# Kernel optimization log

Hardware: AMD Instinct MI355X
Metric: run time of the kernel (lower is better)

Reference implementation:

```python
import jax, jax.numpy as jnp
import numpy as np

N_NODES = 100000
N_EDGES = 1600000
F_IN = 500
HIDDEN = 64
N_CLASS = 40


def gcn_conv(x, W, b, src, dst, n_nodes):
    """PyG GCNConv: add self-loops, symmetric deg^-1/2 normalization,
    linear transform then scatter-add aggregation at dst."""
    h = x @ W  # [N, out]
    loop = jnp.arange(n_nodes, dtype=src.dtype)
    s = jnp.concatenate([src, loop])  # sources incl. self-loops
    d = jnp.concatenate([dst, loop])
    deg = jax.ops.segment_sum(jnp.ones_like(d, dtype=h.dtype), d, num_segments=n_nodes)
    dinv = jnp.where(deg > 0, jax.lax.rsqrt(deg), 0.0)
    norm = dinv[s] * dinv[d]  # [E+N]
    msg = h[s] * norm[:, None]  # gather + scale, [E+N, out]
    out = jax.ops.segment_sum(msg, d, num_segments=n_nodes)
    return out + b


def setup_inputs() -> dict:
    key = jax.random.key(0)
    k1, k2, k3, k4 = jax.random.split(key, 4)
    x = jax.random.normal(k1, (N_NODES, F_IN), dtype=jnp.float32)
    edge_index = jax.random.randint(k2, (2, N_EDGES), 0, N_NODES, dtype=jnp.int64)
    # Glorot-style init for GCNConv weights
    W1 = jax.random.normal(k3, (F_IN, HIDDEN), dtype=jnp.float32) / np.sqrt(F_IN)
    b1 = jnp.zeros((HIDDEN,), dtype=jnp.float32)
    W2 = jax.random.normal(k4, (HIDDEN, N_CLASS), dtype=jnp.float32) / np.sqrt(HIDDEN)
    b2 = jnp.zeros((N_CLASS,), dtype=jnp.float32)
    return {"x": x, "W1": W1, "b1": b1, "W2": W2, "b2": b2, "edge_index": edge_index}


def reference(x, W1, b1, W2, b2, edge_index):
    src, dst = edge_index[0], edge_index[1]
    n = x.shape[0]
    h = jax.nn.relu(gcn_conv(x, W1, b1, src, dst, n))
    # dropout is identity in eval mode (F.dropout with training=False)
    out = gcn_conv(h, W2, b2, src, dst, n)
    return jax.nn.log_softmax(out, axis=1)
```

## Files before the change

### kernel.cpp

```cpp
#include <hip/hip_runtime.h>
#include <math.h>

#define N_NODES 100000
#define N_EDGES 1600000
#define F_IN    500
#define HIDDEN  64
#define N_CLASS 40
#define KPAD    512

#define NB   2048
#define NPB  49
#define EPB  16384
#define CAP  1536

typedef __attribute__((ext_vector_type(4))) float f32x4;
typedef __attribute__((ext_vector_type(8))) __bf16 bf16x8;

__device__ __forceinline__ unsigned short f2bf(float f) {
    unsigned int u = __float_as_uint(f);
    u = (u + 0x7FFF + ((u >> 16) & 1)) >> 16;
    return (unsigned short)u;
}
__device__ __forceinline__ unsigned int packbf(float a, float b) {
    return (unsigned int)f2bf(a) | ((unsigned int)f2bf(b) << 16);
}
__device__ __forceinline__ float bfu_lo(unsigned int v) {
    return __uint_as_float(v << 16);
}
__device__ __forceinline__ float bfu_hi(unsigned int v) {
    return __uint_as_float(v & 0xFFFF0000u);
}

__global__ void k_prep_w1t(const float* __restrict__ w1, unsigned short* __restrict__ w1t,
                           int* __restrict__ bcnt) {
    int idx = blockIdx.x * blockDim.x + threadIdx.x;
    if (idx < NB) bcnt[idx] = 0;
    if (idx >= HIDDEN * KPAD) return;
    int n = idx >> 9, k = idx & (KPAD - 1);
    float v = (k < F_IN) ? w1[k * HIDDEN + n] : 0.f;
    w1t[idx] = f2bf(v);
}

__launch_bounds__(1024)
__global__ void k_bhist(const int* __restrict__ dst, int* __restrict__ bcnt, int e) {
    __shared__ int h[NB];
    for (int i = threadIdx.x; i < NB; i += 1024) h[i] = 0;
    __syncthreads();
    int base = blockIdx.x * EPB;
#pragma unroll
    for (int j = 0; j < 16; ++j) {
        int i = base + j * 1024 + threadIdx.x;
        if (i < e) atomicAdd(&h[dst[i] / NPB], 1);
    }
    __syncthreads();
    for (int i = threadIdx.x; i < NB; i += 1024)
        if (h[i]) atomicAdd(&bcnt[i], h[i]);
}

__launch_bounds__(1024)
__global__ void k_bscan(const int* __restrict__ bcnt, int* __restrict__ bptr,
                        int* __restrict__ bcur) {
    __shared__ int s[1024];
    int t = threadIdx.x;
    int a = bcnt[2 * t], b = bcnt[2 * t + 1];
    int v = a + b;
    s[t] = v;
    __syncthreads();
    for (int off = 1; off < 1024; off <<= 1) {
        int u = (t >= off) ? s[t - off] : 0;
        __syncthreads();
        s[t] += u;
        __syncthreads();
    }
    int excl = s[t] - v;
    bptr[2 * t] = excl;     bptr[2 * t + 1] = excl + a;
    bcur[2 * t] = excl;     bcur[2 * t + 1] = excl + a;
    if (t == 1023) bptr[NB] = s[1023];
}

__launch_bounds__(1024)
__global__ void k_bfill(const int* __restrict__ src, const int* __restrict__ dst,
                        int* __restrict__ bcur, int2* __restrict__ ebuf, int e) {
    __shared__ int hist[NB];
    __shared__ int base_[NB];
    for (int i = threadIdx.x; i < NB; i += 1024) hist[i] = 0;
    __syncthreads();
    int b0 = blockIdx.x * EPB;
    int s_[16], d_[16];
#pragma unroll
    for (int j = 0; j < 16; ++j) {
        int i = b0 + j * 1024 + threadIdx.x;
        if (i < e) {
            s_[j] = src[i];
            d_[j] = dst[i];
            atomicAdd(&hist[d_[j] / NPB], 1);
        } else d_[j] = -1;
    }
    __syncthreads();
    for (int i = threadIdx.x; i < NB; i += 1024) {
        int hc = hist[i];
        base_[i] = hc ? atomicAdd(&bcur[i], hc) : 0;
        hist[i] = 0;
    }
    __syncthreads();
#pragma unroll
    for (int j = 0; j < 16; ++j) {
        if (d_[j] >= 0) {
            int bu = d_[j] / NPB;
            int r = atomicAdd(&hist[bu], 1);
            ebuf[base_[bu] + r] = make_int2(s_[j], d_[j]);
        }
    }
}

__launch_bounds__(256)
__global__ void k_bucket_csr(const int2* __restrict__ ebuf, const int* __restrict__ bptr,
                             int* __restrict__ rp, int* __restrict__ col,
                             float* __restrict__ dinv, int n) {
    int b  = blockIdx.x;
    int lo = b * NPB;
    if (lo >= n) return;
    int hi  = min(lo + NPB, n);
    int eb0 = bptr[b], ec = bptr[b + 1] - eb0;

    __shared__ int2 pairs[CAP];
    __shared__ int  hist[NPB];
    __shared__ int  excl[NPB + 1];
    for (int j = threadIdx.x; j < NPB; j += 256) hist[j] = 0;
    __syncthreads();
    for (int i = threadIdx.x; i < ec; i += 256) {
        int2 p = ebuf[eb0 + i];
        if (i < CAP) pairs[i] = p;
        atomicAdd(&hist[p.y - lo], 1);
    }
    __syncthreads();
    if (threadIdx.x == 0) {
        int acc = 0;
        for (int j = 0; j < NPB; ++j) { excl[j] = acc; acc += hist[j]; }
        excl[NPB] = acc;
    }
    __syncthreads();
    for (int j = threadIdx.x; j < hi - lo; j += 256) {
        rp[lo + j]   = eb0 + excl[j];
        dinv[lo + j] = rsqrtf((float)(hist[j] + 1));
    }
    if (hi == n && threadIdx.x == 0) rp[n] = eb0 + ec;
    __syncthreads();
    for (int j = threadIdx.x; j < NPB; j += 256) hist[j] = 0;
    __syncthreads();
    for (int i = threadIdx.x; i < ec; i += 256) {
        int2 p  = (i < CAP) ? pairs[i] : ebuf[eb0 + i];
        int  li = p.y - lo;
        int  r  = atomicAdd(&hist[li], 1);
        col[eb0 + excl[li] + r] = p.x;
    }
}

__launch_bounds__(512)
__global__ void k_gemm1(const float* __restrict__ x, const unsigned short* __restrict__ w1t,
                        const float* __restrict__ dinv, unsigned short* __restrict__ hs, int n) {
    constexpr int LDW = 520;
    __shared__ __align__(16) unsigned short w1l[HIDDEN * LDW];

    const int tid  = threadIdx.x;
    const int wave = tid >> 6;
    const int lane = tid & 63;
    const int quad = lane >> 4;
    const int l16  = lane & 15;

    {
        const uint4* g = (const uint4*)w1t;
#pragma unroll
        for (int i = 0; i < 8; ++i) {
            int c   = i * 512 + tid;
            int row = c >> 6, cc = c & 63;
            uint4 v = g[c];
            *(uint4*)&w1l[row * LDW + cc * 8] = v;
        }
    }
    __syncthreads();

    const int rowb = blockIdx.x * 128 + wave * 16;
    const int  row = rowb + l16;
    const bool vr  = row < n;
    const float* p = &x[(size_t)(vr ? row : 0) * F_IN];
    const float4 z4 = make_float4(0.f, 0.f, 0.f, 0.f);

    f32x4 acc[4];
#pragma unroll
    for (int ct = 0; ct < 4; ++ct) acc[ct] = (f32x4)0.f;

    float4 xa[8], xb[8];
    auto XLOAD = [&](int ks) {
        const int c0 = ks * 32 + quad * 8;
        if (ks < 15) {
            xa[ks % 8] = vr ? *(const float4*)&p[c0]     : z4;
            xb[ks % 8] = vr ? *(const float4*)&p[c0 + 4] : z4;
        } else {
            const bool cv0 = (c0 + 4 <= F_IN);
            const bool cv1 = (c0 + 8 <= F_IN);
            xa[ks % 8] = (vr && cv0) ? *(const float4*)&p[c0]     : z4;
            xb[ks % 8] = (vr && cv1) ? *(const float4*)&p[c0 + 4] : z4;
        }
    };
#pragma unroll
    for (int ks = 0; ks < 8; ++ks) XLOAD(ks);

#pragma unroll
    for (int ks = 0; ks < 16; ++ks) {
        bf16x8 bfrag[4];
#pragma unroll
        for (int ct = 0; ct < 4; ++ct)
            bfrag[ct] = *(const bf16x8*)&w1l[(ct * 16 + l16) * LDW + ks * 32 + quad * 8];
        const float4 ca = xa[ks % 8];
        const float4 cb = xb[ks % 8];
        if (ks + 8 < 16) XLOAD(ks + 8);
        union { bf16x8 v; unsigned int u[4]; } af;
        af.u[0] = packbf(ca.x, ca.y); af.u[1] = packbf(ca.z, ca.w);
        af.u[2] = packbf(cb.x, cb.y); af.u[3] = packbf(cb.z, cb.w);
#pragma unroll
        for (int ct = 0; ct < 4; ++ct)
            acc[ct] = __builtin_amdgcn_mfma_f32_16x16x32_bf16(af.v, bfrag[ct], acc[ct], 0, 0, 0);
    }

#pragma unroll
    for (int reg = 0; reg < 4; ++reg) {
        int grow = rowb + quad * 4 + reg;
        if (grow < n) {
            float dv = dinv[grow];
#pragma unroll
            for (int ct = 0; ct < 4; ++ct)
                hs[(size_t)grow * HIDDEN + ct * 16 + l16] = f2bf(dv * acc[ct][reg]);
        }
    }
}

template <int F, bool RELU, bool LSM>
__launch_bounds__(256)
__global__ void k_agg(const uint2* __restrict__ hs2, const int* __restrict__ rp,
                      const int* __restrict__ col, const float* __restrict__ dinv,
                      const float* __restrict__ bias, float* __restrict__ out, int n) {
    constexpr int PW2 = F / 4;
    const int lane = threadIdx.x & 63;
    const int q    = lane >> 4;
    const int p    = lane & 15;
    const bool act = p < PW2;
    int wid = __builtin_amdgcn_readfirstlane((blockIdx.x * blockDim.x + threadIdx.x) >> 6);
    const int nw = (gridDim.x * blockDim.x) >> 6;

    for (; wid < n; wid += nw) {
        const int beg = rp[wid], end = rp[wid + 1];
        float a0 = 0.f, a1 = 0.f, a2 = 0.f, a3 = 0.f;
        int e = beg + q;
        for (; e + 12 < end; e += 16) {
            int c0 = col[e], c1 = col[e + 4], c2 = col[e + 8], c3 = col[e + 12];
            uint2 v0 = act ? hs2[(unsigned)c0 * PW2 + p] : make_uint2(0u, 0u);
            uint2 v1 = act ? hs2[(unsigned)c1 * PW2 + p] : make_uint2(0u, 0u);
            uint2 v2 = act ? hs2[(unsigned)c2 * PW2 + p] : make_uint2(0u, 0u);
            uint2 v3 = act ? hs2[(unsigned)c3 * PW2 + p] : make_uint2(0u, 0u);
            a0 += bfu_lo(v0.x) + bfu_lo(v1.x) + bfu_lo(v2.x) + bfu_lo(v3.x);
            a1 += bfu_hi(v0.x) + bfu_hi(v1.x) + bfu_hi(v2.x) + bfu_hi(v3.x);
            a2 += bfu_lo(v0.y) + bfu_lo(v1.y) + bfu_lo(v2.y) + bfu_lo(v3.y);
            a3 += bfu_hi(v0.y) + bfu_hi(v1.y) + bfu_hi(v2.y) + bfu_hi(v3.y);
        }
        if (e + 4 < end) {
            int c0 = col[e], c1 = col[e + 4];
            uint2 v0 = act ? hs2[(unsigned)c0 * PW2 + p] : make_uint2(0u, 0u);
            uint2 v1 = act ? hs2[(unsigned)c1 * PW2 + p] : make_uint2(0u, 0u);
            a0 += bfu_lo(v0.x) + bfu_lo(v1.x);
            a1 += bfu_hi(v0.x) + bfu_hi(v1.x);
            a2 += bfu_lo(v0.y) + bfu_lo(v1.y);
            a3 += bfu_hi(v0.y) + bfu_hi(v1.y);
            e += 8;
        }
        if (e < end) {
            int c0 = col[e];
            uint2 v0 = act ? hs2[(unsigned)c0 * PW2 + p] : make_uint2(0u, 0u);
            a0 += bfu_lo(v0.x); a1 += bfu_hi(v0.x);
            a2 += bfu_lo(v0.y); a3 += bfu_hi(v0.y);
        }
        a0 += __shfl_xor(a0, 16); a1 += __shfl_xor(a1, 16);
        a2 += __shfl_xor(a2, 16); a3 += __shfl_xor(a3, 16);
        a0 += __shfl_xor(a0, 32); a1 += __shfl_xor(a1, 32);
        a2 += __shfl_xor(a2, 32); a3 += __shfl_xor(a3, 32);

        const float di = dinv[wid];
        uint2 sv  = act ? hs2[(unsigned)wid * PW2 + p] : make_uint2(0u, 0u);
        float4 bv = act ? *(const float4*)&bias[4 * p] : make_float4(0.f, 0.f, 0.f, 0.f);
        float r0 = di * (a0 + bfu_lo(sv.x)) + bv.x;
        float r1 = di * (a1 + bfu_hi(sv.x)) + bv.y;
        float r2 = di * (a2 + bfu_lo(sv.y)) + bv.z;
        float r3 = di * (a3 + bfu_hi(sv.y)) + bv.w;
        if (RELU) {
            r0 = fmaxf(r0, 0.f); r1 = fmaxf(r1, 0.f);
            r2 = fmaxf(r2, 0.f); r3 = fmaxf(r3, 0.f);
        }
        if (LSM) {
            float m = act ? fmaxf(fmaxf(r0, r1), fmaxf(r2, r3)) : -INFINITY;
#pragma unroll
            for (int off = 8; off; off >>= 1) m = fmaxf(m, __shfl_xor(m, off));
            float ex = act ? (__expf(r0 - m) + __expf(r1 - m) + __expf(r2 - m) + __expf(r3 - m))
                           : 0.f;
#pragma unroll
            for (int off = 8; off; off >>= 1) ex += __shfl_xor(ex, off);
            float lse = m + __logf(ex);
            r0 -= lse; r1 -= lse; r2 -= lse; r3 -= lse;
        }
        if (q == 0 && act)
            *(float4*)&out[(size_t)wid * F + 4 * p] = make_float4(r0, r1, r2, r3);
    }
}

__launch_bounds__(256)
__global__ void k_gemm2(const float* __restrict__ a, const float* __restrict__ w,
                        const float* __restrict__ dinv, unsigned short* __restrict__ out, int n) {
    __shared__ float ws[HIDDEN * N_CLASS];
    for (int idx = threadIdx.x; idx < HIDDEN * N_CLASS; idx += 256) ws[idx] = w[idx];
    __syncthreads();
    int idx = blockIdx.x * 256 + threadIdx.x;
    if (idx >= n * N_CLASS) return;
    int i = idx / N_CLASS, j = idx - i * N_CLASS;
    float s = 0.f;
#pragma unroll
    for (int k = 0; k < HIDDEN; k += 4) {
        float4 xv = *(const float4*)&a[(size_t)i * HIDDEN + k];
        s = fmaf(xv.x, ws[k * N_CLASS + j], s);
        s = fmaf(xv.y, ws[(k + 1) * N_CLASS + j], s);
        s = fmaf(xv.z, ws[(k + 2) * N_CLASS + j], s);
        s = fmaf(xv.w, ws[(k + 3) * N_CLASS + j], s);
    }
    out[idx] = f2bf(dinv[i] * s);
}

extern "C" void kernel_launch(void* const* d_in, const int* in_sizes, int n_in,
                              void* d_out, int out_size, void* d_ws, size_t ws_size,
                              hipStream_t stream) {
    const float* x   = (const float*)d_in[0];
    const float* W1  = (const float*)d_in[1];
    const float* b1  = (const float*)d_in[2];
    const float* W2  = (const float*)d_in[3];
    const float* b2  = (const float*)d_in[4];
    const int*   ei  = (const int*)d_in[5];
    const int*   src = ei;
    const int*   dst = ei + N_EDGES;
    float*       out = (float*)d_out;

    char*  ws  = (char*)d_ws;
    size_t off = 0;
    auto alloc = [&](size_t bytes) -> void* {
        void* p = ws + off;
        off += (bytes + 255) & ~(size_t)255;
        return p;
    };
    int*            bcnt = (int*)alloc((size_t)NB * 4);
    int*            bptr = (int*)alloc((size_t)(NB + 1) * 4);
    int*            bcur = (int*)alloc((size_t)NB * 4);
    int*            rp   = (int*)alloc((size_t)(N_NODES + 1) * 4);
    int*            col  = (int*)alloc((size_t)N_EDGES * 4);
    float*          dinv = (float*)alloc((size_t)N_NODES * 4);
    unsigned short* w1t  = (unsigned short*)alloc((size_t)HIDDEN * KPAD * 2);
    unsigned short* h1s  = (unsigned short*)alloc((size_t)N_NODES * HIDDEN * 2);
    float*          h1a  = (float*)alloc((size_t)N_NODES * HIDDEN * 4);
    int2*           ebuf = (int2*)h1a;
    unsigned short* h2s  = h1s;

    const int NBH = (N_EDGES + EPB - 1) / EPB;

    k_prep_w1t<<<(HIDDEN * KPAD + 255) / 256, 256, 0, stream>>>(W1, w1t, bcnt);
    k_bhist<<<NBH, 1024, 0, stream>>>(dst, bcnt, N_EDGES);
    k_bscan<<<1, 1024, 0, stream>>>(bcnt, bptr, bcur);
    k_bfill<<<NBH, 1024, 0, stream>>>(src, dst, bcur, ebuf, N_EDGES);
    k_bucket_csr<<<NB, 256, 0, stream>>>(ebuf, bptr, rp, col, dinv, N_NODES);

    k_gemm1<<<(N_NODES + 127) / 128, 512, 0, stream>>>(x, w1t, dinv, h1s, N_NODES);
    k_agg<HIDDEN, true, false><<<2048, 256, 0, stream>>>(
        (const uint2*)h1s, rp, col, dinv, b1, h1a, N_NODES);

    k_gemm2<<<(N_NODES * N_CLASS + 255) / 256, 256, 0, stream>>>(h1a, W2, dinv, h2s, N_NODES);
    k_agg<N_CLASS, false, true><<<2048, 256, 0, stream>>>(
        (const uint2*)h2s, rp, col, dinv, b2, out, N_NODES);
}
```

Before: 514.2 us.

## Stage x tiles into LDS with direct global-to-LDS loads in triple buffer

```diff
diff --git a/kernel.cpp b/kernel.cpp
--- a/kernel.cpp
+++ b/kernel.cpp
@@ -29,6 +29,11 @@
 }
 __device__ __forceinline__ float bfu_hi(unsigned int v) {
     return __uint_as_float(v & 0xFFFF0000u);
+}
+__device__ __forceinline__ void gload_lds16(const void* g, void* l) {
+    __builtin_amdgcn_global_load_lds(
+        (const __attribute__((address_space(1))) unsigned int*)g,
+        (__attribute__((address_space(3))) unsigned int*)l, 16, 0, 0);
 }
 
 __global__ void k_prep_w1t(const float* __restrict__ w1, unsigned short* __restrict__ w1t,
@@ -161,6 +166,7 @@
                         const float* __restrict__ dinv, unsigned short* __restrict__ hs, int n) {
     constexpr int LDW = 520;
     __shared__ __align__(16) unsigned short w1l[HIDDEN * LDW];
+    __shared__ __align__(16) char xs[3][8][2048];
 
     const int tid  = threadIdx.x;
     const int wave = tid >> 6;
@@ -178,46 +184,78 @@
             *(uint4*)&w1l[row * LDW + cc * 8] = v;
         }
     }
-    __syncthreads();
 
     const int rowb = blockIdx.x * 128 + wave * 16;
-    const int  row = rowb + l16;
-    const bool vr  = row < n;
-    const float* p = &x[(size_t)(vr ? row : 0) * F_IN];
-    const float4 z4 = make_float4(0.f, 0.f, 0.f, 0.f);
+
+    const int rloc = lane >> 3;
+    const int csrc = (lane & 7) ^ rloc;
+    int gr0 = rowb + rloc;      if (gr0 > n - 1) gr0 = n - 1;
+    int gr1 = rowb + 8 + rloc;  if (gr1 > n - 1) gr1 = n - 1;
+    const char* sb0 = (const char*)x + (size_t)gr0 * (F_IN * 4) + csrc * 16;
+    const char* sb1 = (const char*)x + (size_t)gr1 * (F_IN * 4) + csrc * 16;
+
+    auto STAGE = [&](int ks) {
+        char* d = &xs[ks % 3][wave][0];
+        gload_lds16(sb0 + ks * 128, d);
+        gload_lds16(sb1 + ks * 128, d + 1024);
+    };
+
+    STAGE(0); STAGE(1);
+    asm volatile("s_waitcnt vmcnt(0)" ::: "memory");
+    __syncthreads();
 
     f32x4 acc[4];
 #pragma unroll
     for (int ct = 0; ct < 4; ++ct) acc[ct] = (f32x4)0.f;
 
-    float4 xa[8], xb[8];
-    auto XLOAD = [&](int ks) {
-        const int c0 = ks * 32 + quad * 8;
-        if (ks < 15) {
-            xa[ks % 8] = vr ? *(const float4*)&p[c0]     : z4;
-            xb[ks % 8] = vr ? *(const float4*)&p[c0 + 4] : z4;
-        } else {
-            const bool cv0 = (c0 + 4 <= F_IN);
-            const bool cv1 = (c0 + 8 <= F_IN);
-            xa[ks % 8] = (vr && cv0) ? *(const float4*)&p[c0]     : z4;
-            xb[ks % 8] = (vr && cv1) ? *(const float4*)&p[c0 + 4] : z4;
-        }
-    };
-#pragma unroll
-    for (int ks = 0; ks < 8; ++ks) XLOAD(ks);
-
-#pragma unroll
-    for (int ks = 0; ks < 16; ++ks) {
+    const int rb  = l16 * 128;
+    const int swz = (l16 & 7) << 4;
+    const int o1  = rb + ((quad * 32) ^ swz);
+    const int o2  = rb + ((quad * 32 + 16) ^ swz);
+
+#pragma unroll
+    for (int ks = 0; ks < 15; ++ks) {
+        if (ks + 2 <= 14) STAGE(ks + 2);
+        if (ks < 13)       asm volatile("s_waitcnt vmcnt(4)" ::: "memory");
+        else if (ks == 13) asm volatile("s_waitcnt vmcnt(2)" ::: "memory");
+        else               asm volatile("s_waitcnt vmcnt(0)" ::: "memory");
+
         bf16x8 bfrag[4];
 #pragma unroll
         for (int ct = 0; ct < 4; ++ct)
             bfrag[ct] = *(const bf16x8*)&w1l[(ct * 16 + l16) * LDW + ks * 32 + quad * 8];
-        const float4 ca = xa[ks % 8];
-        const float4 cb = xb[ks % 8];
-        if (ks + 8 < 16) XLOAD(ks + 8);
+
+        const char* xb = &xs[ks % 3][wave][0];
+        float4 a0 = *(const float4*)(xb + o1);
+        float4 a1 = *(const float4*)(xb + o2);
+
         union { bf16x8 v; unsigned int u[4]; } af;
-        af.u[0] = packbf(ca.x, ca.y); af.u[1] = packbf(ca.z, ca.w);
-        af.u[2] = packbf(cb.x, cb.y); af.u[3] = packbf(cb.z, cb.w);
+        af.u[0] = packbf(a0.x, a0.y); af.u[1] = packbf(a0.z, a0.w);
+        af.u[2] = packbf(a1.x, a1.y); af.u[3] = packbf(a1.z, a1.w);
+#pragma unroll
+        for (int ct = 0; ct < 4; ++ct)
+            acc[ct] = __builtin_amdgcn_mfma_f32_16x16x32_bf16(af.v, bfrag[ct], acc[ct], 0, 0, 0);
+    }
+
+    {
+        const int  row = rowb + l16;
+        const bool vr  = row < n;
+        const float* p = &x[(size_t)(vr ? row : 0) * F_IN];
+        const float4 z4 = make_float4(0.f, 0.f, 0.f, 0.f);
+        const int c0 = 480 + quad * 8;
+        const bool cv0 = (c0 + 4 <= F_IN);
+        const bool cv1 = (c0 + 8 <= F_IN);
+        float4 t0 = (vr && cv0) ? *(const float4*)&p[c0]     : z4;
+        float4 t1 = (vr && cv1) ? *(const float4*)&p[c0 + 4] : z4;
+
+        bf16x8 bfrag[4];
+#pragma unroll
+        for (int ct = 0; ct < 4; ++ct)
+            bfrag[ct] = *(const bf16x8*)&w1l[(ct * 16 + l16) * LDW + 480 + quad * 8];
+
+        union { bf16x8 v; unsigned int u[4]; } af;
+        af.u[0] = packbf(t0.x, t0.y); af.u[1] = packbf(t0.z, t0.w);
+        af.u[2] = packbf(t1.x, t1.y); af.u[3] = packbf(t1.z, t1.w);
 #pragma unroll
         for (int ct = 0; ct < 4; ++ct)
             acc[ct] = __builtin_amdgcn_mfma_f32_16x16x32_bf16(af.v, bfrag[ct], acc[ct], 0, 0, 0);
```

Result: faster. 487.0 us (-5.3%).
